# Performance work log

Measured on AMD Instinct MI355X. Metric: run time of the kernel, lower is better.

The kernel has to match this reference:

```python
import jax, jax.numpy as jnp
import numpy as np

B, N, OBS, ACT = 4, 256, 40, 8
HEAD, DIM = 8, 32
T = HEAD * DIM


def setup_inputs() -> dict:
    key = jax.random.key(0)
    ks = jax.random.split(key, 10)
    x = jax.random.normal(ks[0], (B, N + 1, OBS), dtype=jnp.float32)
    # last row, col 0 carries the (float-encoded) target intersection index
    tgt = jax.random.randint(ks[1], (B,), 0, N)
    x = x.at[:, -1, 0].set(tgt.astype(jnp.float32))
    adj = jax.random.uniform(ks[2], (N, N), dtype=jnp.float32)
    s = 0.02
    return {
        "x": x,
        "adj": adj,
        "We1": jax.random.normal(ks[3], (OBS, T), dtype=jnp.float32) * s,
        "be1": jnp.zeros((T,), jnp.float32),
        "We2": jax.random.normal(ks[4], (T, T), dtype=jnp.float32) * s,
        "be2": jnp.zeros((T,), jnp.float32),
        "Wl": jax.random.normal(ks[5], (T, T), dtype=jnp.float32) * s,
        "bl": jnp.zeros((T,), jnp.float32),
        "Wn": jax.random.normal(ks[6], (T, T), dtype=jnp.float32) * s,
        "bn": jnp.zeros((T,), jnp.float32),
        "Wh": jax.random.normal(ks[7], (T, T), dtype=jnp.float32) * s,
        "bh": jnp.zeros((T,), jnp.float32),
        "Wa": jax.random.normal(ks[8], (DIM, ACT), dtype=jnp.float32) * s,
        "ba": jnp.zeros((ACT,), jnp.float32),
    }


def reference(x, adj, We1, be1, We2, be2, Wl, bl, Wn, bn, Wh, bh, Wa, ba):
    b, np1, _ = x.shape
    n = np1 - 1
    tgt = x[:, -1, 0].astype(jnp.int32)          # [B] target intersection ids
    obs = x[:, :-1, :]                            # [B,N,OBS]
    # obs_embed: Linear+ReLU twice
    emb = jax.nn.relu(obs @ We1 + be1)
    emb = jax.nn.relu(emb @ We2 + be2)            # [B,N,T]
    # tile then matmul by adjacency: result is adj @ emb, replicated along dim 1
    ne = jnp.einsum('mn,bnd->bmd', adj, emb)      # [B,N,T]
    ne = jnp.broadcast_to(ne[:, None], (b, n, n, T))  # [B,N,N,T] (tiled, as in torch)
    # agent heads: [B,N,H,1,D]
    ah = jax.nn.relu(emb @ Wl + bl).reshape(b, n, 1, DIM, HEAD).transpose(0, 1, 4, 2, 3)
    # neighbor heads: [B,N,H,N,D]
    nh = jax.nn.relu(ne @ Wn + bn).reshape(b, n, n, DIM, HEAD).transpose(0, 1, 4, 2, 3)
    # einsum 'ijklm,ijknm->ijklm' with l=1: elementwise over d, summed over n
    attn = ah * nh.sum(axis=3, keepdims=True)     # [B,N,H,1,D]
    attn = jax.nn.softmax(attn, axis=-1)
    hid = jax.nn.relu(ne @ Wh + bh).reshape(b, n, n, DIM, HEAD).transpose(0, 1, 4, 2, 3)
    out = attn * hid.sum(axis=3, keepdims=True)   # [B,N,H,1,D]
    out = out.mean(axis=2).reshape(b, n, DIM)     # mean over heads -> [B,N,D]
    g = out[jnp.arange(b), tgt]                   # gather per-batch target row [B,D]
    act = g @ Wa + ba                             # [B,ACT]
    return act
```

## Files before the change

kernel.cpp:

```cpp
#include <hip/hip_runtime.h>

#define Bsz 4
#define Nn  256
#define OBSD 40
#define ACTD 8
#define HEADS 8
#define DIMD 32
#define Td  256
#define R   4

#define FMA4(accr, s, wv) \
    (accr).x = fmaf((s), (wv).x, (accr).x); \
    (accr).y = fmaf((s), (wv).y, (accr).y); \
    (accr).z = fmaf((s), (wv).z, (accr).z); \
    (accr).w = fmaf((s), (wv).w, (accr).w)

__global__ void k_emb(const float* __restrict__ x,
                      const float* __restrict__ We1, const float* __restrict__ be1,
                      const float* __restrict__ We2, const float* __restrict__ be2,
                      float* __restrict__ emb,
                      float* __restrict__ snh, float* __restrict__ shid) {
    int g = blockIdx.x;
    int t = threadIdx.x;
    int row0 = g * R;
    int b = row0 >> 8;
    int n0 = row0 & 255;
    if (g == 0)      { for (int i = t; i < Bsz * Td; i += 256) snh[i]  = 0.f; }
    else if (g == 1) { for (int i = t; i < Bsz * Td; i += 256) shid[i] = 0.f; }

    __shared__ float4 obs_t[OBSD];
    __shared__ float4 h1_t[Td];
    __shared__ float4 part[4][R][64];
    if (t < R * OBSD) {
        int r = t & (R - 1), k = t >> 2;
        ((float*)&obs_t[k])[r] = x[(b * (Nn + 1) + n0 + r) * OBSD + k];
    }
    __syncthreads();

    float bias1 = be1[t];
    float a1[R] = {bias1, bias1, bias1, bias1};
#pragma unroll
    for (int k = 0; k < OBSD; ++k) {
        float w = We1[k * Td + t];
        float4 ov = obs_t[k];
        a1[0] = fmaf(ov.x, w, a1[0]);
        a1[1] = fmaf(ov.y, w, a1[1]);
        a1[2] = fmaf(ov.z, w, a1[2]);
        a1[3] = fmaf(ov.w, w, a1[3]);
    }
    h1_t[t] = make_float4(fmaxf(a1[0], 0.f), fmaxf(a1[1], 0.f),
                          fmaxf(a1[2], 0.f), fmaxf(a1[3], 0.f));
    __syncthreads();

    int wv = t >> 6, c = t & 63;
    float4 a2[R] = {};
#pragma unroll 8
    for (int i = 0; i < 64; ++i) {
        int k = (wv << 6) + i;
        float4 wvv = *(const float4*)(We2 + k * Td + 4 * c);
        float4 hv = h1_t[k];
        FMA4(a2[0], hv.x, wvv);
        FMA4(a2[1], hv.y, wvv);
        FMA4(a2[2], hv.z, wvv);
        FMA4(a2[3], hv.w, wvv);
    }
#pragma unroll
    for (int r = 0; r < R; ++r) part[wv][r][c] = a2[r];
    __syncthreads();

    int c2 = t >> 2, j = t & 3;
#pragma unroll
    for (int r = 0; r < R; ++r) {
        float v = be2[t];
#pragma unroll
        for (int w2 = 0; w2 < 4; ++w2) v += ((const float*)&part[w2][r][c2])[j];
        emb[(row0 + r) * Td + t] = fmaxf(v, 0.f);
    }
}

__global__ void k_fused(const float* __restrict__ adj, const float* __restrict__ emb,
                        const float* __restrict__ Wn, const float* __restrict__ bn,
                        const float* __restrict__ Wh, const float* __restrict__ bh,
                        float* __restrict__ snh, float* __restrict__ shid) {
    int g = blockIdx.x, b = blockIdx.y;
    int t = threadIdx.x;
    int m0 = g * R;
    __shared__ float4 arow_t[Nn];
    __shared__ float4 nrow_t[Td];
    __shared__ float4 partN[4][R][64];
    __shared__ float4 partH[4][R][64];
    arow_t[t] = make_float4(adj[(m0 + 0) * Nn + t], adj[(m0 + 1) * Nn + t],
                            adj[(m0 + 2) * Nn + t], adj[(m0 + 3) * Nn + t]);
    __syncthreads();

    int wv = t >> 6, c = t & 63;
    const float* eb = emb + b * Nn * Td;

    float4 aN[R] = {};
#pragma unroll 8
    for (int i = 0; i < 64; ++i) {
        int n = (wv << 6) + i;
        float4 ev = *(const float4*)(eb + n * Td + 4 * c);
        float4 ar = arow_t[n];
        FMA4(aN[0], ar.x, ev);
        FMA4(aN[1], ar.y, ev);
        FMA4(aN[2], ar.z, ev);
        FMA4(aN[3], ar.w, ev);
    }
#pragma unroll
    for (int r = 0; r < R; ++r) partN[wv][r][c] = aN[r];
    __syncthreads();

    int c2 = t >> 2, j = t & 3;
    {
        float nr[R];
#pragma unroll
        for (int r = 0; r < R; ++r) {
            float v = 0.f;
#pragma unroll
            for (int w2 = 0; w2 < 4; ++w2) v += ((const float*)&partN[w2][r][c2])[j];
            nr[r] = v;
        }
        nrow_t[t] = make_float4(nr[0], nr[1], nr[2], nr[3]);
    }
    __syncthreads();

    float4 sN[R] = {};
    float4 sH[R] = {};
#pragma unroll 4
    for (int i = 0; i < 64; ++i) {
        int k = (wv << 6) + i;
        float4 nv = nrow_t[k];
        float4 wnv = *(const float4*)(Wn + k * Td + 4 * c);
        float4 whv = *(const float4*)(Wh + k * Td + 4 * c);
        FMA4(sN[0], nv.x, wnv);  FMA4(sH[0], nv.x, whv);
        FMA4(sN[1], nv.y, wnv);  FMA4(sH[1], nv.y, whv);
        FMA4(sN[2], nv.z, wnv);  FMA4(sH[2], nv.z, whv);
        FMA4(sN[3], nv.w, wnv);  FMA4(sH[3], nv.w, whv);
    }
#pragma unroll
    for (int r = 0; r < R; ++r) { partN[wv][r][c] = sN[r]; partH[wv][r][c] = sH[r]; }
    __syncthreads();

    float bnt = bn[t], bht = bh[t];
    float rs1 = 0.f, rs2 = 0.f;
#pragma unroll
    for (int r = 0; r < R; ++r) {
        float v1 = bnt, v2 = bht;
#pragma unroll
        for (int w2 = 0; w2 < 4; ++w2) {
            v1 += ((const float*)&partN[w2][r][c2])[j];
            v2 += ((const float*)&partH[w2][r][c2])[j];
        }
        rs1 += fmaxf(v1, 0.f);
        rs2 += fmaxf(v2, 0.f);
    }
    atomicAdd(&snh[b * Td + t], rs1);
    atomicAdd(&shid[b * Td + t], rs2);
}

__global__ void k_final(const float* __restrict__ x, const float* __restrict__ emb,
                        const float* __restrict__ Wl, const float* __restrict__ bl,
                        const float* __restrict__ snh, const float* __restrict__ shid,
                        const float* __restrict__ Wa, const float* __restrict__ ba,
                        float* __restrict__ out) {
    int b = blockIdx.x;
    int t = threadIdx.x;
    int tgt = (int)x[(b * (Nn + 1) + Nn) * OBSD + 0];
    tgt = tgt < 0 ? 0 : (tgt > Nn - 1 ? Nn - 1 : tgt);
    __shared__ float erow[Td], lg[Td], p[Td], od[DIMD];
    __shared__ float4 partL[4][64];
    erow[t] = emb[(b * Nn + tgt) * Td + t];
    __syncthreads();

    int wv = t >> 6, c = t & 63;
    float4 aL = {};
#pragma unroll 8
    for (int i = 0; i < 64; ++i) {
        int k = (wv << 6) + i;
        float4 wlv = *(const float4*)(Wl + k * Td + 4 * c);
        FMA4(aL, erow[k], wlv);
    }
    partL[wv][c] = aL;
    __syncthreads();

    int c2 = t >> 2, j = t & 3;
    float acc = bl[t];
#pragma unroll
    for (int w2 = 0; w2 < 4; ++w2) acc += ((const float*)&partL[w2][c2])[j];
    float ah = fmaxf(acc, 0.f);
    lg[t] = ah * snh[b * Td + t];
    __syncthreads();
    int h = t & 7;
    float mx = -1e30f;
#pragma unroll
    for (int d = 0; d < DIMD; ++d) mx = fmaxf(mx, lg[d * HEADS + h]);
    float se = 0.f;
#pragma unroll
    for (int d = 0; d < DIMD; ++d) se += __expf(lg[d * HEADS + h] - mx);
    float attn = __expf(lg[t] - mx) / se;
    p[t] = attn * shid[b * Td + t];
    __syncthreads();
    if (t < DIMD) {
        float s = 0.f;
#pragma unroll
        for (int hh = 0; hh < HEADS; ++hh) s += p[t * HEADS + hh];
        od[t] = s * (1.f / HEADS);
    }
    __syncthreads();
    if (t < ACTD) {
        float s = ba[t];
#pragma unroll
        for (int d = 0; d < DIMD; ++d) s = fmaf(od[d], Wa[d * ACTD + t], s);
        out[b * ACTD + t] = s;
    }
}

extern "C" void kernel_launch(void* const* d_in, const int* in_sizes, int n_in,
                              void* d_out, int out_size, void* d_ws, size_t ws_size,
                              hipStream_t stream) {
    const float* x   = (const float*)d_in[0];
    const float* adj = (const float*)d_in[1];
    const float* We1 = (const float*)d_in[2];
    const float* be1 = (const float*)d_in[3];
    const float* We2 = (const float*)d_in[4];
    const float* be2 = (const float*)d_in[5];
    const float* Wl  = (const float*)d_in[6];
    const float* bl  = (const float*)d_in[7];
    const float* Wn  = (const float*)d_in[8];
    const float* bn  = (const float*)d_in[9];
    const float* Wh  = (const float*)d_in[10];
    const float* bh  = (const float*)d_in[11];
    const float* Wa  = (const float*)d_in[12];
    const float* ba  = (const float*)d_in[13];
    float* out = (float*)d_out;

    float* emb  = (float*)d_ws;
    float* snh  = emb + Bsz * Nn * Td;
    float* shid = snh + Bsz * Td;

    k_emb<<<dim3(Bsz * Nn / R), dim3(Td), 0, stream>>>(x, We1, be1, We2, be2, emb, snh, shid);
    k_fused<<<dim3(Nn / R, Bsz), dim3(Td), 0, stream>>>(adj, emb, Wn, bn, Wh, bh, snh, shid);
    k_final<<<dim3(Bsz), dim3(Td), 0, stream>>>(x, emb, Wl, bl, snh, shid, Wa, ba, out);
}
```

Before: 109.3 us.

## Split fused adjacency/projection kernel and halve rows per block

The fused adj@emb plus Wn/Wh projection kernel is split in two. k_ne computes the adjacency product with 2 rows per block and writes a full NE buffer to workspace. k_colsum then projects 4 NE rows per block through Wn and Wh and accumulates the column sums atomically. k_emb also drops to 2 rows per block, doubling its grid. The aim is more blocks for occupancy on the many CUs, at the cost of an extra launch, an NE round trip through global memory, and more reloads of the weights.

```diff
diff --git a/kernel.cpp b/kernel.cpp
--- a/kernel.cpp
+++ b/kernel.cpp
@@ -7,7 +7,6 @@
 #define HEADS 8
 #define DIMD 32
 #define Td  256
-#define R   4
 
 #define FMA4(accr, s, wv) \
     (accr).x = fmaf((s), (wv).x, (accr).x); \
@@ -22,55 +21,50 @@
                       float* __restrict__ snh, float* __restrict__ shid) {
     int g = blockIdx.x;
     int t = threadIdx.x;
-    int row0 = g * R;
+    int row0 = g * 2;
     int b = row0 >> 8;
     int n0 = row0 & 255;
     if (g == 0)      { for (int i = t; i < Bsz * Td; i += 256) snh[i]  = 0.f; }
     else if (g == 1) { for (int i = t; i < Bsz * Td; i += 256) shid[i] = 0.f; }
 
-    __shared__ float4 obs_t[OBSD];
-    __shared__ float4 h1_t[Td];
-    __shared__ float4 part[4][R][64];
-    if (t < R * OBSD) {
-        int r = t & (R - 1), k = t >> 2;
+    __shared__ float2 obs_t[OBSD];
+    __shared__ float2 h1_t[Td];
+    __shared__ float4 part[4][2][64];
+    if (t < 2 * OBSD) {
+        int r = t & 1, k = t >> 1;
         ((float*)&obs_t[k])[r] = x[(b * (Nn + 1) + n0 + r) * OBSD + k];
     }
     __syncthreads();
 
     float bias1 = be1[t];
-    float a1[R] = {bias1, bias1, bias1, bias1};
+    float a10 = bias1, a11 = bias1;
 #pragma unroll
     for (int k = 0; k < OBSD; ++k) {
         float w = We1[k * Td + t];
-        float4 ov = obs_t[k];
-        a1[0] = fmaf(ov.x, w, a1[0]);
-        a1[1] = fmaf(ov.y, w, a1[1]);
-        a1[2] = fmaf(ov.z, w, a1[2]);
-        a1[3] = fmaf(ov.w, w, a1[3]);
-    }
-    h1_t[t] = make_float4(fmaxf(a1[0], 0.f), fmaxf(a1[1], 0.f),
-                          fmaxf(a1[2], 0.f), fmaxf(a1[3], 0.f));
-    __syncthreads();
-
-    int wv = t >> 6, c = t & 63;
-    float4 a2[R] = {};
+        float2 ov = obs_t[k];
+        a10 = fmaf(ov.x, w, a10);
+        a11 = fmaf(ov.y, w, a11);
+    }
+    h1_t[t] = make_float2(fmaxf(a10, 0.f), fmaxf(a11, 0.f));
+    __syncthreads();
+
+    int wv = t >> 6, c = t & 63;
+    float4 a2[2] = {};
 #pragma unroll 8
     for (int i = 0; i < 64; ++i) {
         int k = (wv << 6) + i;
         float4 wvv = *(const float4*)(We2 + k * Td + 4 * c);
-        float4 hv = h1_t[k];
+        float2 hv = h1_t[k];
         FMA4(a2[0], hv.x, wvv);
         FMA4(a2[1], hv.y, wvv);
-        FMA4(a2[2], hv.z, wvv);
-        FMA4(a2[3], hv.w, wvv);
-    }
-#pragma unroll
-    for (int r = 0; r < R; ++r) part[wv][r][c] = a2[r];
-    __syncthreads();
-
-    int c2 = t >> 2, j = t & 3;
-#pragma unroll
-    for (int r = 0; r < R; ++r) {
+    }
+    part[wv][0][c] = a2[0];
+    part[wv][1][c] = a2[1];
+    __syncthreads();
+
+    int c2 = t >> 2, j = t & 3;
+#pragma unroll
+    for (int r = 0; r < 2; ++r) {
         float v = be2[t];
 #pragma unroll
         for (int w2 = 0; w2 < 4; ++w2) v += ((const float*)&part[w2][r][c2])[j];
@@ -78,74 +72,79 @@
     }
 }
 
-__global__ void k_fused(const float* __restrict__ adj, const float* __restrict__ emb,
-                        const float* __restrict__ Wn, const float* __restrict__ bn,
-                        const float* __restrict__ Wh, const float* __restrict__ bh,
-                        float* __restrict__ snh, float* __restrict__ shid) {
+__global__ void k_ne(const float* __restrict__ adj, const float* __restrict__ emb,
+                     float* __restrict__ NE) {
     int g = blockIdx.x, b = blockIdx.y;
     int t = threadIdx.x;
-    int m0 = g * R;
-    __shared__ float4 arow_t[Nn];
-    __shared__ float4 nrow_t[Td];
-    __shared__ float4 partN[4][R][64];
-    __shared__ float4 partH[4][R][64];
-    arow_t[t] = make_float4(adj[(m0 + 0) * Nn + t], adj[(m0 + 1) * Nn + t],
-                            adj[(m0 + 2) * Nn + t], adj[(m0 + 3) * Nn + t]);
+    int m0 = g * 2;
+    __shared__ float2 arow_t[Nn];
+    __shared__ float4 part[4][2][64];
+    arow_t[t] = make_float2(adj[(m0 + 0) * Nn + t], adj[(m0 + 1) * Nn + t]);
     __syncthreads();
 
     int wv = t >> 6, c = t & 63;
     const float* eb = emb + b * Nn * Td;
-
-    float4 aN[R] = {};
+    float4 aN[2] = {};
 #pragma unroll 8
     for (int i = 0; i < 64; ++i) {
         int n = (wv << 6) + i;
         float4 ev = *(const float4*)(eb + n * Td + 4 * c);
-        float4 ar = arow_t[n];
+        float2 ar = arow_t[n];
         FMA4(aN[0], ar.x, ev);
         FMA4(aN[1], ar.y, ev);
-        FMA4(aN[2], ar.z, ev);
-        FMA4(aN[3], ar.w, ev);
-    }
-#pragma unroll
-    for (int r = 0; r < R; ++r) partN[wv][r][c] = aN[r];
-    __syncthreads();
-
-    int c2 = t >> 2, j = t & 3;
-    {
-        float nr[R];
-#pragma unroll
-        for (int r = 0; r < R; ++r) {
-            float v = 0.f;
-#pragma unroll
-            for (int w2 = 0; w2 < 4; ++w2) v += ((const float*)&partN[w2][r][c2])[j];
-            nr[r] = v;
-        }
-        nrow_t[t] = make_float4(nr[0], nr[1], nr[2], nr[3]);
-    }
-    __syncthreads();
-
-    float4 sN[R] = {};
-    float4 sH[R] = {};
-#pragma unroll 4
+    }
+    part[wv][0][c] = aN[0];
+    part[wv][1][c] = aN[1];
+    __syncthreads();
+
+    int c2 = t >> 2, j = t & 3;
+#pragma unroll
+    for (int r = 0; r < 2; ++r) {
+        float v = 0.f;
+#pragma unroll
+        for (int w2 = 0; w2 < 4; ++w2) v += ((const float*)&part[w2][r][c2])[j];
+        NE[(b * Nn + m0 + r) * Td + t] = v;
+    }
+}
+
+__global__ void k_colsum(const float* __restrict__ NE,
+                         const float* __restrict__ Wn, const float* __restrict__ bn,
+                         const float* __restrict__ Wh, const float* __restrict__ bh,
+                         float* __restrict__ snh, float* __restrict__ shid) {
+    int g = blockIdx.x, b = blockIdx.y;
+    int t = threadIdx.x;
+    int j0 = g * 4;
+    __shared__ float4 ne4[Td];
+    __shared__ float4 partN[4][4][64];
+    __shared__ float4 partH[4][4][64];
+#pragma unroll
+    for (int r = 0; r < 4; ++r)
+        ((float*)&ne4[t])[r] = NE[(b * Nn + j0 + r) * Td + t];
+    __syncthreads();
+
+    int wv = t >> 6, c = t & 63;
+    float4 sN[4] = {};
+    float4 sH[4] = {};
+#pragma unroll 8
     for (int i = 0; i < 64; ++i) {
         int k = (wv << 6) + i;
-        float4 nv = nrow_t[k];
-        float4 wnv = *(const float4*)(Wn + k * Td + 4 * c);
-        float4 whv = *(const float4*)(Wh + k * Td + 4 * c);
-        FMA4(sN[0], nv.x, wnv);  FMA4(sH[0], nv.x, whv);
-        FMA4(sN[1], nv.y, wnv);  FMA4(sH[1], nv.y, whv);
-        FMA4(sN[2], nv.z, wnv);  FMA4(sH[2], nv.z, whv);
-        FMA4(sN[3], nv.w, wnv);  FMA4(sH[3], nv.w, whv);
-    }
-#pragma unroll
-    for (int r = 0; r < R; ++r) { partN[wv][r][c] = sN[r]; partH[wv][r][c] = sH[r]; }
-    __syncthreads();
-
+        float4 nv = ne4[k];
+        float4 wn4 = *(const float4*)(Wn + k * Td + 4 * c);
+        float4 wh4 = *(const float4*)(Wh + k * Td + 4 * c);
+        FMA4(sN[0], nv.x, wn4);  FMA4(sH[0], nv.x, wh4);
+        FMA4(sN[1], nv.y, wn4);  FMA4(sH[1], nv.y, wh4);
+        FMA4(sN[2], nv.z, wn4);  FMA4(sH[2], nv.z, wh4);
+        FMA4(sN[3], nv.w, wn4);  FMA4(sH[3], nv.w, wh4);
+    }
+#pragma unroll
+    for (int r = 0; r < 4; ++r) { partN[wv][r][c] = sN[r]; partH[wv][r][c] = sH[r]; }
+    __syncthreads();
+
+    int c2 = t >> 2, j = t & 3;
     float bnt = bn[t], bht = bh[t];
     float rs1 = 0.f, rs2 = 0.f;
 #pragma unroll
-    for (int r = 0; r < R; ++r) {
+    for (int r = 0; r < 4; ++r) {
         float v1 = bnt, v2 = bht;
 #pragma unroll
         for (int w2 = 0; w2 < 4; ++w2) {
@@ -236,10 +235,12 @@
     float* out = (float*)d_out;
 
     float* emb  = (float*)d_ws;
-    float* snh  = emb + Bsz * Nn * Td;
+    float* NE   = emb + Bsz * Nn * Td;
+    float* snh  = NE + Bsz * Nn * Td;
     float* shid = snh + Bsz * Td;
 
-    k_emb<<<dim3(Bsz * Nn / R), dim3(Td), 0, stream>>>(x, We1, be1, We2, be2, emb, snh, shid);
-    k_fused<<<dim3(Nn / R, Bsz), dim3(Td), 0, stream>>>(adj, emb, Wn, bn, Wh, bh, snh, shid);
+    k_emb<<<dim3(Bsz * Nn / 2), dim3(Td), 0, stream>>>(x, We1, be1, We2, be2, emb, snh, shid);
+    k_ne<<<dim3(Nn / 2, Bsz), dim3(Td), 0, stream>>>(adj, emb, NE);
+    k_colsum<<<dim3(Nn / 4, Bsz), dim3(Td), 0, stream>>>(NE, Wn, bn, Wh, bh, snh, shid);
     k_final<<<dim3(Bsz), dim3(Td), 0, stream>>>(x, emb, Wl, bl, snh, shid, Wa, ba, out);
 }
```

Result: slower. 122.3 us (+11.9%).
